# Kernel tuning notes

Hardware: AMD Instinct MI355X
Metric: run time of the kernel (lower is better)

The kernel has to match this reference:

```python
import jax, jax.numpy as jnp
import numpy as np

HEAD_SIZE = 64
NEG_INF = float('-inf')


def setup_inputs() -> dict:
    key = jax.random.key(0)
    ks = jax.random.split(key, 4)
    B, S, H, D = 8, 4096, 1024, HEAD_SIZE
    scale = 1.0 / np.sqrt(H)
    return {
        'x': jax.random.normal(ks[0], (B, S, H), dtype=jnp.float32),
        'Wq': jax.random.normal(ks[1], (H, D), dtype=jnp.float32) * scale,
        'bq': jnp.zeros((D,), dtype=jnp.float32),
        'Wk': jax.random.normal(ks[2], (H, D), dtype=jnp.float32) * scale,
        'bk': jnp.zeros((D,), dtype=jnp.float32),
        'Wv': jax.random.normal(ks[3], (H, D), dtype=jnp.float32) * scale,
        'bv': jnp.zeros((D,), dtype=jnp.float32),
    }


def reference(x, Wq, bq, Wk, bk, Wv, bv):
    # x: [B, S, H]; projections -> [B, S, D]
    B, S, H = x.shape
    q = jnp.einsum('bsh,hd->bsd', x, Wq) + bq
    k = jnp.einsum('bsh,hd->bsd', x, Wk) + bk
    v = jnp.einsum('bsh,hd->bsd', x, Wv) + bv
    # raw scores [B, S, S]
    scores = jnp.einsum('bqd,bkd->bqk', q, k)
    # causal mask applied BEFORE scaling (matches original; -inf/scale == -inf)
    causal = jnp.tril(jnp.ones((S, S), dtype=bool))
    scores = jnp.where(causal, scores, NEG_INF)
    scale = 1.0 / jnp.sqrt(jnp.asarray(q.shape[-1], dtype=scores.dtype))
    attn = jax.nn.softmax(scores * scale, axis=-1)
    # dropout = 0.0 (eval) -> identity
    return jnp.einsum('bqk,bkd->bqd', attn, v)
```

## Files before the change

kernel.cpp:

```cpp
#include <hip/hip_runtime.h>
#include <hip/hip_bf16.h>
#include <math.h>

#define SEQ 4096
#define HID 1024
#define DH  64
#define NB  8
#define QSCALE 0.18033688011112042f

typedef unsigned short ushort_t;
typedef unsigned int   uint_t;
typedef __attribute__((ext_vector_type(8))) short  bf16x8;
typedef __attribute__((ext_vector_type(4))) float  f32x4;
typedef __attribute__((ext_vector_type(4))) uint_t u32x4;
typedef __attribute__((ext_vector_type(2))) uint_t u32x2;

static __device__ __forceinline__ ushort_t f2bf(float f) {
    __hip_bfloat16 h = __float2bfloat16(f);
    return *reinterpret_cast<ushort_t*>(&h);
}
static __device__ __forceinline__ ushort_t f2bf_fast(float f) {
    uint_t u = __float_as_uint(f);
    return (ushort_t)((u + 0x8000u) >> 16);
}
static __device__ __forceinline__ uint_t bfpair(float lo, float hi) {
    return (uint_t)f2bf_fast(lo) | ((uint_t)f2bf_fast(hi) << 16);
}

static __device__ __forceinline__ void gld_lds16(const void* g, void* s) {
    __builtin_amdgcn_global_load_lds(
        (const __attribute__((address_space(1))) void*)g,
        (__attribute__((address_space(3))) void*)s, 16, 0, 0);
}

__global__ __launch_bounds__(256) void prep_w(
    const float* __restrict__ Wq, const float* __restrict__ Wk,
    const float* __restrict__ Wv, ushort_t* __restrict__ wts)
{
    __shared__ ushort_t tr[64][72];
    const int bx   = blockIdx.x;
    const int mmat = bx >> 4;
    const int kt   = bx & 15;
    const float* W  = (mmat == 0) ? Wq : (mmat == 1) ? Wk : Wv;
    const float  sc = (mmat == 0) ? QSCALE : 1.0f;

    const int t  = threadIdx.x;
    const int kr = t >> 2, kc = (t & 3) * 16;
    const float* src = W + (size_t)(kt * 64 + kr) * DH + kc;
    float4 a0 = *(const float4*)(src);
    float4 a1 = *(const float4*)(src + 4);
    float4 a2 = *(const float4*)(src + 8);
    float4 a3 = *(const float4*)(src + 12);
    float vv[16] = {a0.x,a0.y,a0.z,a0.w, a1.x,a1.y,a1.z,a1.w,
                    a2.x,a2.y,a2.z,a2.w, a3.x,a3.y,a3.z,a3.w};
    #pragma unroll
    for (int i = 0; i < 16; ++i) tr[kr][kc + i] = f2bf(vv[i] * sc);
    __syncthreads();

    const int cl = t >> 2, jc = (t & 3) * 16;
    const int c  = mmat * 64 + cl;
    ushort_t* dst = wts + kt * 12288 + c * 64;
    #pragma unroll
    for (int jj = 0; jj < 16; ++jj) {
        int j = jc + jj;
        dst[((j >> 3) ^ (cl & 7)) * 8 + (j & 7)] = tr[j][cl];
    }
}

__global__ __launch_bounds__(256) void qkv_proj(
    const float* __restrict__ x, const ushort_t* __restrict__ wts,
    const float* __restrict__ bq, const float* __restrict__ bk,
    const float* __restrict__ bv,
    ushort_t* __restrict__ qimg, ushort_t* __restrict__ kimg,
    ushort_t* __restrict__ vimg)
{
    __shared__ ushort_t xs[2][64][72];
    __shared__ ushort_t bw[2][12288];

    const int t  = threadIdx.x;
    const int w  = t >> 6, l = t & 63, lr = l & 15, lg = l >> 4;
    const int row0 = blockIdx.x * 64;
    const int sxr = t >> 2, sxc = (t & 3) * 16;
    const int ch0 = (lg ^ (lr & 7)) * 8;
    const int ch1 = ((lg + 4) ^ (lr & 7)) * 8;

    f32x4 acc[4][3];
    #pragma unroll
    for (int i = 0; i < 4; ++i)
        #pragma unroll
        for (int j = 0; j < 3; ++j) acc[i][j] = (f32x4){0.f,0.f,0.f,0.f};

    const char* wbase = (const char*)wts;
    const int   wlo   = w * 1024 + l * 16;

    float4 Xf[4];
    {
        const float* xr = x + (size_t)(row0 + sxr) * HID + sxc;
        Xf[0] = *(const float4*)(xr);      Xf[1] = *(const float4*)(xr + 4);
        Xf[2] = *(const float4*)(xr + 8);  Xf[3] = *(const float4*)(xr + 12);
        char* bdst = (char*)&bw[0][0] + w * 1024;
        #pragma unroll
        for (int i = 0; i < 6; ++i)
            gld_lds16(wbase + wlo + i * 4096, bdst + i * 4096);
    }

    for (int kt = 0; kt < 16; ++kt) {
        const int buf = kt & 1;
        {
            u32x4 p0, p1;
            p0.x = bfpair(Xf[0].x, Xf[0].y);
            p0.y = bfpair(Xf[0].z, Xf[0].w);
            p0.z = bfpair(Xf[1].x, Xf[1].y);
            p0.w = bfpair(Xf[1].z, Xf[1].w);
            p1.x = bfpair(Xf[2].x, Xf[2].y);
            p1.y = bfpair(Xf[2].z, Xf[2].w);
            p1.z = bfpair(Xf[3].x, Xf[3].y);
            p1.w = bfpair(Xf[3].z, Xf[3].w);
            *(u32x4*)&xs[buf][sxr][sxc]     = p0;
            *(u32x4*)&xs[buf][sxr][sxc + 8] = p1;
        }
        __syncthreads();
        if (kt < 15) {
            const float* xr = x + (size_t)(row0 + sxr) * HID + (kt + 1) * 64 + sxc;
            Xf[0] = *(const float4*)(xr);      Xf[1] = *(const float4*)(xr + 4);
            Xf[2] = *(const float4*)(xr + 8);  Xf[3] = *(const float4*)(xr + 12);
            char* bdst = (char*)&bw[buf ^ 1][0] + w * 1024;
            const char* bsrc = wbase + (size_t)(kt + 1) * 24576 + wlo;
            #pragma unroll
            for (int i = 0; i < 6; ++i)
                gld_lds16(bsrc + i * 4096, bdst + i * 4096);
        }
        bf16x8 af0[4], af1[4];
        #pragma unroll
        for (int rt = 0; rt < 4; ++rt) {
            af0[rt] = *(bf16x8*)&xs[buf][rt * 16 + lr][lg * 8];
            af1[rt] = *(bf16x8*)&xs[buf][rt * 16 + lr][lg * 8 + 32];
        }
        #pragma unroll
        for (int ctl = 0; ctl < 3; ++ctl) {
            const int c = (w * 3 + ctl) * 16 + lr;
            bf16x8 b0 = *(bf16x8*)&bw[buf][c * 64 + ch0];
            bf16x8 b1 = *(bf16x8*)&bw[buf][c * 64 + ch1];
            #pragma unroll
            for (int rt = 0; rt < 4; ++rt) {
                acc[rt][ctl] = __builtin_amdgcn_mfma_f32_16x16x32_bf16(
                    af0[rt], b0, acc[rt][ctl], 0, 0, 0);
                acc[rt][ctl] = __builtin_amdgcn_mfma_f32_16x16x32_bf16(
                    af1[rt], b1, acc[rt][ctl], 0, 0, 0);
            }
        }
    }

    #pragma unroll
    for (int ctl = 0; ctl < 3; ++ctl) {
        const int c    = (w * 3 + ctl) * 16 + lr;
        const int mmat = c >> 6;
        const int cc   = c & 63;
        const float* bp = (mmat == 0) ? bq : (mmat == 1) ? bk : bv;
        const float bias = bp[cc] * (mmat == 0 ? QSCALE : 1.0f);
        #pragma unroll
        for (int rt = 0; rt < 4; ++rt)
            #pragma unroll
            for (int r = 0; r < 4; ++r) {
                const int s = row0 + rt * 16 + lg * 4 + r;
                const ushort_t v = f2bf_fast(acc[rt][ctl][r] + bias);
                if (mmat == 0)
                    qimg[(size_t)s * 64 + cc] = v;
                else if (mmat == 1)
                    kimg[(size_t)(s >> 6) * 4096 + (s & 63) * 64 +
                         ((cc >> 3) ^ (s & 7)) * 8 + (cc & 7)] = v;
                else
                    vimg[(size_t)(s >> 6) * 4096 + (size_t)cc * 64 +
                         (((s & 63) >> 3) ^ (cc & 7)) * 8 + (s & 7)] = v;
            }
    }
}

__global__ __launch_bounds__(256) void attn(
    const ushort_t* __restrict__ qimg, const ushort_t* __restrict__ kimg,
    const ushort_t* __restrict__ vimg,
    float* __restrict__ Opart, float* __restrict__ Lpart)
{
    __shared__ ushort_t kvs[2][8192];
    __shared__ ushort_t ps[64][72];

    const int t  = threadIdx.x;
    const int w  = t >> 6, l = t & 63, lr = l & 15, g = l >> 4;
    const int bx   = blockIdx.x;
    const int half = bx & 1;
    const int u    = bx >> 1;
    const int qt   = 63 - (u >> 3);
    const int b    = u & 7;
    const int q0   = qt * 64;
    const int n    = qt + 1, h = n >> 1;
    const int t0   = half ? h : 0;
    const int t1   = half ? n : h;
    const int ch0 = (g ^ (lr & 7)) * 8;
    const int ch1 = ((g + 4) ^ (lr & 7)) * 8;
    const int qq  = q0 + w * 16 + lr;

    bf16x8 qf0, qf1;
    {
        const ushort_t* qp = qimg + (size_t)(b * SEQ + qq) * 64 + g * 8;
        qf0 = *(const bf16x8*)(qp);
        qf1 = *(const bf16x8*)(qp + 32);
    }

    f32x4 o[4];
    #pragma unroll
    for (int dt = 0; dt < 4; ++dt) o[dt] = (f32x4){0.f,0.f,0.f,0.f};
    float lpart = 0.f;

    const char* kbase = (const char*)kimg + (size_t)b * 524288;
    const char* vbase = (const char*)vimg + (size_t)b * 524288;
    const int wo = w * 1024;
    const int lo = l * 16;

    if (t0 < t1) {
        const char* ks = kbase + (size_t)t0 * 8192;
        const char* vs = vbase + (size_t)t0 * 8192;
        char* lk = (char*)&kvs[0][0];
        gld_lds16(ks + wo + lo,        lk + wo);
        gld_lds16(ks + wo + lo + 4096, lk + wo + 4096);
        gld_lds16(vs + wo + lo,        lk + wo + 8192);
        gld_lds16(vs + wo + lo + 4096, lk + wo + 12288);
    }

    for (int kt = t0; kt < t1; ++kt) {
        const int cur = (kt - t0) & 1;
        __syncthreads();
        if (kt + 1 < t1) {
            const char* ks = kbase + (size_t)(kt + 1) * 8192;
            const char* vs = vbase + (size_t)(kt + 1) * 8192;
            char*       lk = (char*)&kvs[cur ^ 1][0];
            gld_lds16(ks + wo + lo,        lk + wo);
            gld_lds16(ks + wo + lo + 4096, lk + wo + 4096);
            gld_lds16(vs + wo + lo,        lk + wo + 8192);
            gld_lds16(vs + wo + lo + 4096, lk + wo + 12288);
        }

        const ushort_t* kb = &kvs[cur][0];
        f32x4 s[4];
        #pragma unroll
        for (int ct = 0; ct < 4; ++ct) {
            const int rowb = (ct * 16 + lr) * 64;
            bf16x8 kf0 = *(const bf16x8*)(kb + rowb + ch0);
            bf16x8 kf1 = *(const bf16x8*)(kb + rowb + ch1);
            s[ct] = (f32x4){0.f,0.f,0.f,0.f};
            s[ct] = __builtin_amdgcn_mfma_f32_16x16x32_bf16(kf0, qf0, s[ct], 0, 0, 0);
            s[ct] = __builtin_amdgcn_mfma_f32_16x16x32_bf16(kf1, qf1, s[ct], 0, 0, 0);
        }

        if (kt == qt) {
            const int kvb = kt * 64 + g * 4;
            #pragma unroll
            for (int ct = 0; ct < 4; ++ct) {
                float p0 = ((kvb + ct*16 + 0) > qq) ? 0.f : __builtin_amdgcn_exp2f(s[ct][0]);
                float p1 = ((kvb + ct*16 + 1) > qq) ? 0.f : __builtin_amdgcn_exp2f(s[ct][1]);
                float p2 = ((kvb + ct*16 + 2) > qq) ? 0.f : __builtin_amdgcn_exp2f(s[ct][2]);
                float p3 = ((kvb + ct*16 + 3) > qq) ? 0.f : __builtin_amdgcn_exp2f(s[ct][3]);
                lpart += (p0 + p1) + (p2 + p3);
                u32x2 pk = { bfpair(p0, p1), bfpair(p2, p3) };
                *(u32x2*)&ps[w * 16 + lr][ct * 16 + g * 4] = pk;
            }
        } else {
            #pragma unroll
            for (int ct = 0; ct < 4; ++ct) {
                float p0 = __builtin_amdgcn_exp2f(s[ct][0]);
                float p1 = __builtin_amdgcn_exp2f(s[ct][1]);
                float p2 = __builtin_amdgcn_exp2f(s[ct][2]);
                float p3 = __builtin_amdgcn_exp2f(s[ct][3]);
                lpart += (p0 + p1) + (p2 + p3);
                u32x2 pk = { bfpair(p0, p1), bfpair(p2, p3) };
                *(u32x2*)&ps[w * 16 + lr][ct * 16 + g * 4] = pk;
            }
        }
        asm volatile("s_waitcnt lgkmcnt(0)" ::: "memory");

        bf16x8 pf0 = *(const bf16x8*)&ps[w * 16 + lr][g * 8];
        bf16x8 pf1 = *(const bf16x8*)&ps[w * 16 + lr][32 + g * 8];
        const ushort_t* vb = &kvs[cur][4096];
        #pragma unroll
        for (int dt = 0; dt < 4; ++dt) {
            const int rowb = (dt * 16 + lr) * 64;
            bf16x8 vf0 = *(const bf16x8*)(vb + rowb + ch0);
            bf16x8 vf1 = *(const bf16x8*)(vb + rowb + ch1);
            o[dt] = __builtin_amdgcn_mfma_f32_16x16x32_bf16(vf0, pf0, o[dt], 0, 0, 0);
            o[dt] = __builtin_amdgcn_mfma_f32_16x16x32_bf16(vf1, pf1, o[dt], 0, 0, 0);
        }
    }

    lpart += __shfl_xor(lpart, 16);
    lpart += __shfl_xor(lpart, 32);

    const int m = b * 64 + qt;
    float* Op = Opart + ((size_t)half * 512 + m) * 4096;
    #pragma unroll
    for (int dt = 0; dt < 4; ++dt)
        *(f32x4*)&Op[(w * 16 + lr) * 64 + dt * 16 + g * 4] = o[dt];
    if (g == 0)
        Lpart[((size_t)half * 512 + m) * 64 + w * 16 + lr] = lpart;
}

__global__ __launch_bounds__(256) void merge_o(
    const float* __restrict__ Opart, const float* __restrict__ Lpart,
    float* __restrict__ outg)
{
    const int m = blockIdx.x;
    const int b = m >> 6, qt = m & 63;
    const int t = threadIdx.x;
    const int row = t >> 2, c = (t & 3) * 16;

    const float* A = Opart + (size_t)m * 4096 + row * 64 + c;
    const float* B = Opart + (size_t)(512 + m) * 4096 + row * 64 + c;
    const float la = Lpart[(size_t)m * 64 + row];
    const float lb = Lpart[(size_t)(512 + m) * 64 + row];
    const float inv = 1.0f / (la + lb);
    float* dst = outg + ((size_t)b * SEQ + qt * 64 + row) * 64 + c;
    #pragma unroll
    for (int j = 0; j < 4; ++j) {
        float4 va = *(const float4*)(A + j * 4);
        float4 vb = *(const float4*)(B + j * 4);
        float4 vo = { (va.x + vb.x) * inv, (va.y + vb.y) * inv,
                      (va.z + vb.z) * inv, (va.w + vb.w) * inv };
        *(float4*)(dst + j * 4) = vo;
    }
}

extern "C" void kernel_launch(void* const* d_in, const int* in_sizes, int n_in,
                              void* d_out, int out_size, void* d_ws, size_t ws_size,
                              hipStream_t stream) {
    const float* x  = (const float*)d_in[0];
    const float* Wq = (const float*)d_in[1];
    const float* bq = (const float*)d_in[2];
    const float* Wk = (const float*)d_in[3];
    const float* bk = (const float*)d_in[4];
    const float* Wv = (const float*)d_in[5];
    const float* bv = (const float*)d_in[6];
    float* out = (float*)d_out;

    const size_t per = (size_t)NB * SEQ * DH;
    ushort_t* q   = (ushort_t*)d_ws;
    ushort_t* k   = q + per;
    ushort_t* v   = k + per;
    ushort_t* wts = v + per;
    float* Opart  = (float*)((char*)d_ws + (size_t)(16u << 20));
    float* Lpart  = (float*)((char*)d_ws + (size_t)(40u << 20));

    prep_w  <<<dim3(48),   256, 0, stream>>>(Wq, Wk, Wv, wts);
    qkv_proj<<<dim3(512),  256, 0, stream>>>(x, wts, bq, bk, bv, q, k, v);
    attn    <<<dim3(1024), 256, 0, stream>>>(q, k, v, Opart, Lpart);
    merge_o <<<dim3(512),  256, 0, stream>>>(Opart, Lpart, out);
}
```

Before: 259.0 us.

## Repartition QKV projection so each wave owns 16 rows, loading x straight to registers

The QKV projection kernel now gives each wave a 16-row slice of x and all 192 output columns, instead of all 64 rows and a 48-column slice. Each lane loads and converts its own x fragment directly into MFMA operand registers, so the x shared-memory staging buffer and its store/load round trip are gone. The cost is that every wave must read all 12 column tiles of the weight buffer from LDS, multiplying weight LDS reads, while x is read from global memory in a less coalesced pattern.

```diff
diff --git a/kernel.cpp b/kernel.cpp
--- a/kernel.cpp
+++ b/kernel.cpp
@@ -74,30 +74,29 @@
     ushort_t* __restrict__ qimg, ushort_t* __restrict__ kimg,
     ushort_t* __restrict__ vimg)
 {
-    __shared__ ushort_t xs[2][64][72];
     __shared__ ushort_t bw[2][12288];
 
     const int t  = threadIdx.x;
-    const int w  = t >> 6, l = t & 63, lr = l & 15, lg = l >> 4;
+    const int w  = t >> 6, l = t & 63, lr = l & 15, g = l >> 4;
     const int row0 = blockIdx.x * 64;
-    const int sxr = t >> 2, sxc = (t & 3) * 16;
-    const int ch0 = (lg ^ (lr & 7)) * 8;
-    const int ch1 = ((lg + 4) ^ (lr & 7)) * 8;
-
-    f32x4 acc[4][3];
-    #pragma unroll
-    for (int i = 0; i < 4; ++i)
-        #pragma unroll
-        for (int j = 0; j < 3; ++j) acc[i][j] = (f32x4){0.f,0.f,0.f,0.f};
+    const int row  = row0 + w * 16 + lr;
+    const int ch0 = (g ^ (lr & 7)) * 8;
+    const int ch1 = ((g + 4) ^ (lr & 7)) * 8;
+
+    f32x4 acc[12];
+    #pragma unroll
+    for (int i = 0; i < 12; ++i) acc[i] = (f32x4){0.f,0.f,0.f,0.f};
 
     const char* wbase = (const char*)wts;
     const int   wlo   = w * 1024 + l * 16;
-
-    float4 Xf[4];
+    const float* xrow = x + (size_t)row * HID + g * 8;
+
+    float4 Xa0, Xa1, Xb0, Xb1;
     {
-        const float* xr = x + (size_t)(row0 + sxr) * HID + sxc;
-        Xf[0] = *(const float4*)(xr);      Xf[1] = *(const float4*)(xr + 4);
-        Xf[2] = *(const float4*)(xr + 8);  Xf[3] = *(const float4*)(xr + 12);
+        Xa0 = *(const float4*)(xrow);
+        Xa1 = *(const float4*)(xrow + 4);
+        Xb0 = *(const float4*)(xrow + 32);
+        Xb1 = *(const float4*)(xrow + 36);
         char* bdst = (char*)&bw[0][0] + w * 1024;
         #pragma unroll
         for (int i = 0; i < 6; ++i)
@@ -106,73 +105,62 @@
 
     for (int kt = 0; kt < 16; ++kt) {
         const int buf = kt & 1;
-        {
-            u32x4 p0, p1;
-            p0.x = bfpair(Xf[0].x, Xf[0].y);
-            p0.y = bfpair(Xf[0].z, Xf[0].w);
-            p0.z = bfpair(Xf[1].x, Xf[1].y);
-            p0.w = bfpair(Xf[1].z, Xf[1].w);
-            p1.x = bfpair(Xf[2].x, Xf[2].y);
-            p1.y = bfpair(Xf[2].z, Xf[2].w);
-            p1.z = bfpair(Xf[3].x, Xf[3].y);
-            p1.w = bfpair(Xf[3].z, Xf[3].w);
-            *(u32x4*)&xs[buf][sxr][sxc]     = p0;
-            *(u32x4*)&xs[buf][sxr][sxc + 8] = p1;
-        }
         __syncthreads();
+        float4 Na0, Na1, Nb0, Nb1;
         if (kt < 15) {
-            const float* xr = x + (size_t)(row0 + sxr) * HID + (kt + 1) * 64 + sxc;
-            Xf[0] = *(const float4*)(xr);      Xf[1] = *(const float4*)(xr + 4);
-            Xf[2] = *(const float4*)(xr + 8);  Xf[3] = *(const float4*)(xr + 12);
+            const float* xn = xrow + (kt + 1) * 64;
+            Na0 = *(const float4*)(xn);
+            Na1 = *(const float4*)(xn + 4);
+            Nb0 = *(const float4*)(xn + 32);
+            Nb1 = *(const float4*)(xn + 36);
             char* bdst = (char*)&bw[buf ^ 1][0] + w * 1024;
             const char* bsrc = wbase + (size_t)(kt + 1) * 24576 + wlo;
             #pragma unroll
             for (int i = 0; i < 6; ++i)
                 gld_lds16(bsrc + i * 4096, bdst + i * 4096);
         }
-        bf16x8 af0[4], af1[4];
-        #pragma unroll
-        for (int rt = 0; rt < 4; ++rt) {
-            af0[rt] = *(bf16x8*)&xs[buf][rt * 16 + lr][lg * 8];
-            af1[rt] = *(bf16x8*)&xs[buf][rt * 16 + lr][lg * 8 + 32];
-        }
-        #pragma unroll
-        for (int ctl = 0; ctl < 3; ++ctl) {
-            const int c = (w * 3 + ctl) * 16 + lr;
+        bf16x8 af0, af1;
+        {
+            u32x4 p;
+            p.x = bfpair(Xa0.x, Xa0.y); p.y = bfpair(Xa0.z, Xa0.w);
+            p.z = bfpair(Xa1.x, Xa1.y); p.w = bfpair(Xa1.z, Xa1.w);
+            af0 = *(bf16x8*)&p;
+            u32x4 q;
+            q.x = bfpair(Xb0.x, Xb0.y); q.y = bfpair(Xb0.z, Xb0.w);
+            q.z = bfpair(Xb1.x, Xb1.y); q.w = bfpair(Xb1.z, Xb1.w);
+            af1 = *(bf16x8*)&q;
+        }
+        #pragma unroll
+        for (int ct = 0; ct < 12; ++ct) {
+            const int c = ct * 16 + lr;
             bf16x8 b0 = *(bf16x8*)&bw[buf][c * 64 + ch0];
             bf16x8 b1 = *(bf16x8*)&bw[buf][c * 64 + ch1];
-            #pragma unroll
-            for (int rt = 0; rt < 4; ++rt) {
-                acc[rt][ctl] = __builtin_amdgcn_mfma_f32_16x16x32_bf16(
-                    af0[rt], b0, acc[rt][ctl], 0, 0, 0);
-                acc[rt][ctl] = __builtin_amdgcn_mfma_f32_16x16x32_bf16(
-                    af1[rt], b1, acc[rt][ctl], 0, 0, 0);
-            }
-        }
-    }
-
-    #pragma unroll
-    for (int ctl = 0; ctl < 3; ++ctl) {
-        const int c    = (w * 3 + ctl) * 16 + lr;
+            acc[ct] = __builtin_amdgcn_mfma_f32_16x16x32_bf16(af0, b0, acc[ct], 0, 0, 0);
+            acc[ct] = __builtin_amdgcn_mfma_f32_16x16x32_bf16(af1, b1, acc[ct], 0, 0, 0);
+        }
+        Xa0 = Na0; Xa1 = Na1; Xb0 = Nb0; Xb1 = Nb1;
+    }
+
+    #pragma unroll
+    for (int ct = 0; ct < 12; ++ct) {
+        const int c    = ct * 16 + lr;
         const int mmat = c >> 6;
         const int cc   = c & 63;
         const float* bp = (mmat == 0) ? bq : (mmat == 1) ? bk : bv;
         const float bias = bp[cc] * (mmat == 0 ? QSCALE : 1.0f);
         #pragma unroll
-        for (int rt = 0; rt < 4; ++rt)
-            #pragma unroll
-            for (int r = 0; r < 4; ++r) {
-                const int s = row0 + rt * 16 + lg * 4 + r;
-                const ushort_t v = f2bf_fast(acc[rt][ctl][r] + bias);
-                if (mmat == 0)
-                    qimg[(size_t)s * 64 + cc] = v;
-                else if (mmat == 1)
-                    kimg[(size_t)(s >> 6) * 4096 + (s & 63) * 64 +
-                         ((cc >> 3) ^ (s & 7)) * 8 + (cc & 7)] = v;
-                else
-                    vimg[(size_t)(s >> 6) * 4096 + (size_t)cc * 64 +
-                         (((s & 63) >> 3) ^ (cc & 7)) * 8 + (s & 7)] = v;
-            }
+        for (int r = 0; r < 4; ++r) {
+            const int s = row0 + w * 16 + g * 4 + r;
+            const ushort_t v = f2bf_fast(acc[ct][r] + bias);
+            if (mmat == 0)
+                qimg[(size_t)s * 64 + cc] = v;
+            else if (mmat == 1)
+                kimg[(size_t)(s >> 6) * 4096 + (s & 63) * 64 +
+                     ((cc >> 3) ^ (s & 7)) * 8 + (cc & 7)] = v;
+            else
+                vimg[(size_t)(s >> 6) * 4096 + (size_t)cc * 64 +
+                     (((s & 63) >> 3) ^ (cc & 7)) * 8 + (s & 7)] = v;
+        }
     }
 }
 
```

New measurement: 258.9 us. No clear change (-0.0%).
